# Optimization experiments

Measured on AMD Instinct MI355X. Metric: run time of the kernel, lower is better.

Reference implementation:

```python
import jax, jax.numpy as jnp
import numpy as np
import math

D = 768
H = 12
HD = D // H  # 64
B, N = 16, 1024
EPS = 1e-5


def _rope(x, cos, sin):
    # x: [B,N,H,hd]; cos,sin: [1,N,1,hd]
    x1, x2 = x[..., ::2], x[..., 1::2]
    return jnp.concatenate(
        [x1 * cos[..., ::2] - x2 * sin[..., ::2],
         x1 * sin[..., 1::2] + x2 * cos[..., 1::2]], axis=-1)


def setup_inputs() -> dict:
    key = jax.random.key(0)
    ks = jax.random.split(key, 8)
    s = 1.0 / math.sqrt(D)  # xavier-ish scale
    return {
        "x": jax.random.normal(ks[0], (B, N, D), jnp.float32),
        "rope_emb": jax.random.normal(ks[1], (N, HD), jnp.float32),
        "ln_w": jnp.ones((D,), jnp.float32),
        "ln_b": jnp.zeros((D,), jnp.float32),
        "enc_w": jax.random.normal(ks[2], (D, D), jnp.float32) * s,
        "enc_b": jnp.zeros((D,), jnp.float32),
        "qk_w": jax.random.normal(ks[3], (D, D), jnp.float32) * s,
        "qk_b": jnp.zeros((D,), jnp.float32),
        "v_w": jax.random.normal(ks[4], (D, D), jnp.float32) * s,
        "v_b": jnp.zeros((D,), jnp.float32),
        "out_w": jax.random.normal(ks[5], (D, D), jnp.float32) * s,
        "out_b": jnp.zeros((D,), jnp.float32),
        "gate_w": jax.random.normal(ks[6], (D, D), jnp.float32) * s,
        "gate_b": jnp.zeros((D,), jnp.float32),
    }


def reference(x, rope_emb, ln_w, ln_b, enc_w, enc_b, qk_w, qk_b,
              v_w, v_b, out_w, out_b, gate_w, gate_b):
    b, n, d = x.shape
    # Pre-LayerNorm
    mu = jnp.mean(x, axis=-1, keepdims=True)
    var = jnp.mean(jnp.square(x - mu), axis=-1, keepdims=True)
    x_norm = (x - mu) / jnp.sqrt(var + EPS) * ln_w + ln_b
    # sparse latent encoder
    x_latent = jax.nn.relu(x_norm @ enc_w.T + enc_b)
    qk = (x_latent @ qk_w.T + qk_b).reshape(b, n, H, HD)
    v = (x_latent @ v_w.T + v_b).reshape(b, n, H, HD)
    ang = rope_emb[:, :HD]
    cos = jnp.cos(ang)[None, :, None, :]
    sin = jnp.sin(ang)[None, :, None, :]
    qk = _rope(qk, cos, sin)
    # raw (softmax-free) attention, Q=K
    scores = jnp.einsum('bnhd,bmhd->bhnm', qk, qk) / math.sqrt(HD)
    attn = jnp.einsum('bhnm,bmhd->bnhd', scores, v).reshape(b, n, d)
    attn = attn @ out_w.T + out_b
    gate = jax.nn.sigmoid(x_norm @ gate_w.T + gate_b)
    return x + gate * attn
```

## Files before the change

kernel.cpp:

```cpp
#include <hip/hip_runtime.h>

typedef __bf16 bf16;
typedef __bf16 bf16x4 __attribute__((ext_vector_type(4)));
typedef __bf16 bf16x8 __attribute__((ext_vector_type(8)));
typedef float floatx4 __attribute__((ext_vector_type(4)));

#define DD 768
#define NH 12
#define HDIM 64
#define BB 16
#define NN 1024
#define MTOT (BB*NN)
#define WELEM (DD*DD)

__device__ __forceinline__ void async_cp16(const void* g, void* l) {
  __builtin_amdgcn_global_load_lds((const __attribute__((address_space(1))) void*)g,
                                   (__attribute__((address_space(3))) void*)l, 16, 0, 0);
}

__global__ __launch_bounds__(256) void ln_kernel(const float* __restrict__ x,
    const float* __restrict__ w, const float* __restrict__ b, bf16* __restrict__ A) {
  int row = blockIdx.x * 4 + (threadIdx.x >> 6);
  int lane = threadIdx.x & 63;
  const float4* xr = (const float4*)(x + (size_t)row * DD);
  float4 v[3];
  float s = 0.f;
#pragma unroll
  for (int i = 0; i < 3; i++) {
    v[i] = xr[lane + 64 * i];
    s += v[i].x + v[i].y + v[i].z + v[i].w;
  }
#pragma unroll
  for (int o = 32; o; o >>= 1) s += __shfl_xor(s, o);
  float mu = s * (1.f / 768.f);
  float vs = 0.f;
#pragma unroll
  for (int i = 0; i < 3; i++) {
    float dx;
    dx = v[i].x - mu; vs += dx * dx;
    dx = v[i].y - mu; vs += dx * dx;
    dx = v[i].z - mu; vs += dx * dx;
    dx = v[i].w - mu; vs += dx * dx;
  }
#pragma unroll
  for (int o = 32; o; o >>= 1) vs += __shfl_xor(vs, o);
  float rstd = rsqrtf(vs * (1.f / 768.f) + 1e-5f);
  const float4* wv = (const float4*)w;
  const float4* bv = (const float4*)b;
  bf16* Ar = A + (size_t)row * DD;
#pragma unroll
  for (int i = 0; i < 3; i++) {
    int c4 = lane + 64 * i;
    float4 ww = wv[c4], bb = bv[c4];
    bf16x4 pk;
    pk[0] = (bf16)((v[i].x - mu) * rstd * ww.x + bb.x);
    pk[1] = (bf16)((v[i].y - mu) * rstd * ww.y + bb.y);
    pk[2] = (bf16)((v[i].z - mu) * rstd * ww.z + bb.z);
    pk[3] = (bf16)((v[i].w - mu) * rstd * ww.w + bb.w);
    *(bf16x4*)(Ar + c4 * 4) = pk;
  }
}

__global__ __launch_bounds__(256) void convw_kernel(const float* __restrict__ w0,
    const float* __restrict__ w1, const float* __restrict__ w2,
    const float* __restrict__ w3, const float* __restrict__ w4, bf16* __restrict__ out) {
  int i = blockIdx.x * 256 + threadIdx.x;
  int which = i / (WELEM / 4);
  int off = (i % (WELEM / 4)) * 4;
  const float* s = which == 0 ? w0 : which == 1 ? w1 : which == 2 ? w2 : which == 3 ? w3 : w4;
  float4 v = *(const float4*)(s + off);
  bf16x4 pk;
  pk[0] = (bf16)v.x; pk[1] = (bf16)v.y; pk[2] = (bf16)v.z; pk[3] = (bf16)v.w;
  *(bf16x4*)(out + (size_t)i * 4) = pk;
}

template<int EPI>
__device__ __forceinline__ void gemm_body(
    int bm, int bn, int bnl,
    const bf16* __restrict__ Aop, const bf16* __restrict__ W,
    const float* __restrict__ bias,
    bf16* __restrict__ Cb, float* __restrict__ Cf,
    const float* __restrict__ Xres, const bf16* __restrict__ Gate,
    bf16* As, bf16* Bs) {
  int tid = threadIdx.x;
  int wave = tid >> 6, lane = tid & 63;
  int quad = lane >> 4, l16 = lane & 15;
  int wm = wave & 1, wn = wave >> 1;
  int sr = lane >> 3;
  int smcg = (lane & 7) ^ sr;

  const bf16* Ag = Aop + (size_t)(bm * 256) * DD;
  const bf16* Bg = W + (size_t)(bn * 128) * DD;

  floatx4 acc[8][4];
#pragma unroll
  for (int i = 0; i < 8; i++)
#pragma unroll
    for (int j = 0; j < 4; j++)
      acc[i][j] = (floatx4){0.f, 0.f, 0.f, 0.f};

  int swzA = (l16 & 7);

  for (int k0 = 0; k0 < DD; k0 += 64) {
    __syncthreads();
#pragma unroll
    for (int it = 0; it < 8; it++) {
      int c = it * 4 + wave;
      int row = c * 8 + sr;
      async_cp16(Ag + (size_t)row * DD + k0 + smcg * 8, &As[c * 512]);
    }
#pragma unroll
    for (int it = 0; it < 4; it++) {
      int c = it * 4 + wave;
      int row = c * 8 + sr;
      async_cp16(Bg + (size_t)row * DD + k0 + smcg * 8, &Bs[c * 512]);
    }
    __syncthreads();
#pragma unroll
    for (int ks = 0; ks < 2; ks++) {
      int cg = (ks * 4 + quad) ^ swzA;
      bf16x8 a[8], b[4];
#pragma unroll
      for (int i = 0; i < 8; i++) a[i] = *(const bf16x8*)&As[(wm * 128 + i * 16 + l16) * 64 + cg * 8];
#pragma unroll
      for (int i = 0; i < 4; i++) b[i] = *(const bf16x8*)&Bs[(wn * 64 + i * 16 + l16) * 64 + cg * 8];
      if (EPI == 2) {
#pragma unroll
        for (int mi = 0; mi < 8; mi++)
#pragma unroll
          for (int ni = 0; ni < 4; ni++)
            acc[mi][ni] = __builtin_amdgcn_mfma_f32_16x16x32_bf16(a[mi], b[ni], acc[mi][ni], 0, 0, 0);
      } else {
#pragma unroll
        for (int mi = 0; mi < 8; mi++)
#pragma unroll
          for (int ni = 0; ni < 4; ni++)
            acc[mi][ni] = __builtin_amdgcn_mfma_f32_16x16x32_bf16(b[ni], a[mi], acc[mi][ni], 0, 0, 0);
      }
    }
  }

  if (EPI == 2) {
#pragma unroll
    for (int ni = 0; ni < 4; ni++) {
      int gc = bnl * 128 + wn * 64 + ni * 16 + l16;
      float bz = bias[gc];
      int h = gc >> 6, dd2 = gc & 63;
#pragma unroll
      for (int mi = 0; mi < 8; mi++) {
        int gm0 = bm * 256 + wm * 128 + mi * 16 + quad * 4;
        int b_ = gm0 >> 10, n0 = gm0 & 1023;
        bf16x4 pk;
#pragma unroll
        for (int r = 0; r < 4; r++) pk[r] = (bf16)(acc[mi][ni][r] + bz);
        *(bf16x4*)&Cb[(((size_t)b_ * NH + h) * HDIM + dd2) * NN + n0] = pk;
      }
    }
  } else {
#pragma unroll
    for (int mi = 0; mi < 8; mi++) {
      int gm = bm * 256 + wm * 128 + mi * 16 + l16;
#pragma unroll
      for (int ni = 0; ni < 4; ni++) {
        int gc = bnl * 128 + wn * 64 + ni * 16 + quad * 4;
        float4 bz = *(const float4*)&bias[gc];
        float v0 = acc[mi][ni][0] + bz.x;
        float v1 = acc[mi][ni][1] + bz.y;
        float v2 = acc[mi][ni][2] + bz.z;
        float v3 = acc[mi][ni][3] + bz.w;
        size_t idx = (size_t)gm * DD + gc;
        if (EPI == 4) {
          bf16x4 g = *(const bf16x4*)&Gate[idx];
          float4 xr = *(const float4*)&Xres[idx];
          float4 o;
          o.x = xr.x + (float)g[0] * v0;
          o.y = xr.y + (float)g[1] * v1;
          o.z = xr.z + (float)g[2] * v2;
          o.w = xr.w + (float)g[3] * v3;
          *(float4*)&Cf[idx] = o;
        } else {
          bf16x4 pk;
          if (EPI == 0) {
            pk[0] = (bf16)fmaxf(v0, 0.f); pk[1] = (bf16)fmaxf(v1, 0.f);
            pk[2] = (bf16)fmaxf(v2, 0.f); pk[3] = (bf16)fmaxf(v3, 0.f);
          } else if (EPI == 1) {
            pk[0] = (bf16)v0; pk[1] = (bf16)v1; pk[2] = (bf16)v2; pk[3] = (bf16)v3;
          } else {
            pk[0] = (bf16)(1.f / (1.f + __expf(-v0)));
            pk[1] = (bf16)(1.f / (1.f + __expf(-v1)));
            pk[2] = (bf16)(1.f / (1.f + __expf(-v2)));
            pk[3] = (bf16)(1.f / (1.f + __expf(-v3)));
          }
          *(bf16x4*)&Cb[idx] = pk;
        }
      }
    }
  }
}

template<int EPI_LO, int EPI_HI, int NBN>
__global__ __launch_bounds__(256, 2) void gemm_kernel(
    const bf16* __restrict__ Aop, const bf16* __restrict__ W,
    const float* __restrict__ bias_lo, const float* __restrict__ bias_hi,
    bf16* __restrict__ C_lo, bf16* __restrict__ C_hi, float* __restrict__ Cf,
    const float* __restrict__ Xres, const bf16* __restrict__ Gate) {
  __shared__ bf16 As[256 * 64];
  __shared__ bf16 Bs[128 * 64];
  int blk = blockIdx.x;
  int xcd = blk & 7, slot = blk >> 3;
  int bm = xcd * 8 + slot / NBN;
  int bn = slot % NBN;
  if (NBN == 12 && bn >= 6) {
    gemm_body<EPI_HI>(bm, bn, bn - 6, Aop, W, bias_hi, C_hi, Cf, Xres, Gate, As, Bs);
  } else {
    gemm_body<EPI_LO>(bm, bn, bn, Aop, W, bias_lo, C_lo, Cf, Xres, Gate, As, Bs);
  }
}

#define TLS_S 132
__global__ __launch_bounds__(256) void rope_kernel(const bf16* __restrict__ QKraw,
    const float* __restrict__ rope, bf16* __restrict__ QKr, bf16* __restrict__ QKrT) {
  __shared__ bf16 Tls[64 * TLS_S];
  int blk = blockIdx.x;
  int bh = blk >> 3, nc = blk & 7;
  int b_ = bh / NH, h_ = bh % NH;
  int nbase = nc * 128;
  int t = threadIdx.x;
  {
    int n_loc = t >> 1, ch = t & 1;
    int n = nbase + n_loc;
    const bf16* src = QKraw + ((size_t)(b_ * NN + n)) * DD + h_ * HDIM + ch * 32;
    const float* rp = rope + n * HDIM + ch * 32;
    __attribute__((aligned(16))) bf16 o1[16];
    __attribute__((aligned(16))) bf16 o2[16];
#pragma unroll
    for (int i0 = 0; i0 < 4; i0++) {
      bf16x8 v = *(const bf16x8*)(src + i0 * 8);
      float4 r0 = *(const float4*)(rp + i0 * 8);
      float4 r1 = *(const float4*)(rp + i0 * 8 + 4);
      float a0s[4] = {r0.x, r0.z, r1.x, r1.z};
      float a1s[4] = {r0.y, r0.w, r1.y, r1.w};
#pragma unroll
      for (int p = 0; p < 4; p++) {
        float x1 = (float)v[2 * p], x2 = (float)v[2 * p + 1];
        float s0, c0, s1, c1;
        __sincosf(a0s[p], &s0, &c0);
        __sincosf(a1s[p], &s1, &c1);
        int d = i0 * 4 + p;
        o1[d] = (bf16)(x1 * c0 - x2 * s0);
        o2[d] = (bf16)(x1 * s1 + x2 * c1);
      }
    }
    bf16* dst = QKr + ((size_t)(b_ * NN + n)) * DD + h_ * HDIM;
    *(bf16x8*)&dst[ch * 16]      = *(bf16x8*)&o1[0];
    *(bf16x8*)&dst[ch * 16 + 8]  = *(bf16x8*)&o1[8];
    *(bf16x8*)&dst[32 + ch * 16]     = *(bf16x8*)&o2[0];
    *(bf16x8*)&dst[32 + ch * 16 + 8] = *(bf16x8*)&o2[8];
#pragma unroll
    for (int d = 0; d < 16; d++) {
      Tls[(ch * 16 + d) * TLS_S + n_loc] = o1[d];
      Tls[(32 + ch * 16 + d) * TLS_S + n_loc] = o2[d];
    }
  }
  __syncthreads();
  {
    int c = t >> 2, qn = t & 3;
    __attribute__((aligned(16))) bf16 buf[32];
#pragma unroll
    for (int j = 0; j < 8; j++)
      *(bf16x4*)&buf[j * 4] = *(const bf16x4*)&Tls[c * TLS_S + qn * 32 + j * 4];
    bf16* dst = QKrT + ((size_t)bh * HDIM + c) * NN + nbase + qn * 32;
#pragma unroll
    for (int j = 0; j < 4; j++)
      *(bf16x8*)&dst[j * 8] = *(bf16x8*)&buf[j * 8];
  }
}

__global__ __launch_bounds__(256) void attn_kernel(const bf16* __restrict__ QKr,
    const bf16* __restrict__ QKrT, const bf16* __restrict__ VT, bf16* __restrict__ attn) {
  __shared__ float Tp[64][64];
  __shared__ bf16 Tbf[64][72];
  int blk = blockIdx.x;
  int xcd = blk & 7, s = blk >> 3;
  int bhl = s >> 2, q = s & 3;
  int bh = xcd * 24 + bhl;
  int tid = threadIdx.x, wave = tid >> 6, lane = tid & 63;
  int quad = lane >> 4, l16 = lane & 15;
  const bf16* Qt = QKrT + (size_t)bh * (HDIM * NN);
  const bf16* Vt = VT + (size_t)bh * (HDIM * NN);

  floatx4 acc[4][4];
#pragma unroll
  for (int i = 0; i < 4; i++)
#pragma unroll
    for (int j = 0; j < 4; j++)
      acc[i][j] = (floatx4){0.f, 0.f, 0.f, 0.f};

  int kbase = wave * 256;
#pragma unroll
  for (int k0 = 0; k0 < 256; k0 += 32) {
    bf16x8 a[4], b[4];
#pragma unroll
    for (int i = 0; i < 4; i++) a[i] = *(const bf16x8*)&Qt[(size_t)(i * 16 + l16) * NN + kbase + k0 + quad * 8];
#pragma unroll
    for (int i = 0; i < 4; i++) b[i] = *(const bf16x8*)&Vt[(size_t)(i * 16 + l16) * NN + kbase + k0 + quad * 8];
#pragma unroll
    for (int mi = 0; mi < 4; mi++)
#pragma unroll
      for (int ni = 0; ni < 4; ni++)
        acc[mi][ni] = __builtin_amdgcn_mfma_f32_16x16x32_bf16(a[mi], b[ni], acc[mi][ni], 0, 0, 0);
  }
#pragma unroll
  for (int w = 0; w < 4; w++) {
    if (wave == w) {
#pragma unroll
      for (int mi = 0; mi < 4; mi++)
#pragma unroll
        for (int ni = 0; ni < 4; ni++)
#pragma unroll
          for (int r = 0; r < 4; r++) {
            float val = acc[mi][ni][r];
            float* p = &Tp[mi * 16 + quad * 4 + r][ni * 16 + l16];
            if (w == 0) *p = val; else *p += val;
          }
    }
    __syncthreads();
  }
  for (int e = tid; e < 4096; e += 256) {
    int d1 = e >> 6, d2 = e & 63;
    Tbf[d2][d1] = (bf16)(Tp[d1][d2] * 0.125f);
  }
  __syncthreads();

  int b_ = bh / NH, h_ = bh % NH;
  const bf16* Q = QKr + (size_t)(b_ * NN) * DD + h_ * HDIM;
  bf16* Ao = attn + (size_t)(b_ * NN) * DD + h_ * HDIM;
  bf16x8 Bf[4][2];
#pragma unroll
  for (int ni = 0; ni < 4; ni++)
#pragma unroll
    for (int ks = 0; ks < 2; ks++)
      Bf[ni][ks] = *(const bf16x8*)&Tbf[ni * 16 + l16][ks * 32 + quad * 8];

#pragma unroll
  for (int mi = 0; mi < 4; mi++) {
    int nrow = q * 256 + wave * 64 + mi * 16;
    bf16x8 a0 = *(const bf16x8*)&Q[(size_t)(nrow + l16) * DD + quad * 8];
    bf16x8 a1 = *(const bf16x8*)&Q[(size_t)(nrow + l16) * DD + 32 + quad * 8];
    floatx4 o[4];
#pragma unroll
    for (int ni = 0; ni < 4; ni++) o[ni] = (floatx4){0.f, 0.f, 0.f, 0.f};
#pragma unroll
    for (int ni = 0; ni < 4; ni++) {
      o[ni] = __builtin_amdgcn_mfma_f32_16x16x32_bf16(a0, Bf[ni][0], o[ni], 0, 0, 0);
      o[ni] = __builtin_amdgcn_mfma_f32_16x16x32_bf16(a1, Bf[ni][1], o[ni], 0, 0, 0);
    }
#pragma unroll
    for (int ni = 0; ni < 4; ni++)
#pragma unroll
      for (int r = 0; r < 4; r++)
        Ao[(size_t)(nrow + quad * 4 + r) * DD + ni * 16 + l16] = (bf16)o[ni][r];
  }
}

extern "C" void kernel_launch(void* const* d_in, const int* in_sizes, int n_in,
                              void* d_out, int out_size, void* d_ws, size_t ws_size,
                              hipStream_t stream) {
  const float* x      = (const float*)d_in[0];
  const float* rope   = (const float*)d_in[1];
  const float* ln_w   = (const float*)d_in[2];
  const float* ln_b   = (const float*)d_in[3];
  const float* enc_w  = (const float*)d_in[4];
  const float* enc_b  = (const float*)d_in[5];
  const float* qk_w   = (const float*)d_in[6];
  const float* qk_b   = (const float*)d_in[7];
  const float* v_w    = (const float*)d_in[8];
  const float* v_b    = (const float*)d_in[9];
  const float* out_w  = (const float*)d_in[10];
  const float* out_b  = (const float*)d_in[11];
  const float* gate_w = (const float*)d_in[12];
  const float* gate_b = (const float*)d_in[13];

  char* w = (char*)d_ws;
  const size_t S = (size_t)MTOT * DD * 2;
  bf16* s0 = (bf16*)(w);
  bf16* s1 = (bf16*)(w + S);
  bf16* s2 = (bf16*)(w + 2 * S);
  bf16* s3 = (bf16*)(w + 3 * S);
  bf16* s4 = (bf16*)(w + 4 * S);
  bf16* s5 = (bf16*)(w + 5 * S);
  bf16* Wb = (bf16*)(w + 6 * S);

  bf16* A = s0;
  bf16* L = s1;
  bf16* Gate = s2;
  bf16* QKraw = s0;
  bf16* QKr = s3;
  bf16* QKrT = s4;
  bf16* VT = s5;
  bf16* attnb = s1;

  ln_kernel<<<dim3(MTOT / 4), dim3(256), 0, stream>>>(x, ln_w, ln_b, A);
  convw_kernel<<<dim3(5 * WELEM / 4 / 256), dim3(256), 0, stream>>>(enc_w, gate_w, qk_w, v_w, out_w, Wb);

  gemm_kernel<0, 3, 12><<<dim3(768), dim3(256), 0, stream>>>(
      A, Wb, enc_b, gate_b, L, Gate, nullptr, nullptr, nullptr);
  gemm_kernel<1, 2, 12><<<dim3(768), dim3(256), 0, stream>>>(
      L, Wb + 2 * (size_t)WELEM, qk_b, v_b, QKraw, VT, nullptr, nullptr, nullptr);
  rope_kernel<<<dim3(BB * NH * 8), dim3(256), 0, stream>>>(QKraw, rope, QKr, QKrT);
  attn_kernel<<<dim3(BB * NH * 4), dim3(256), 0, stream>>>(QKr, QKrT, VT, attnb);
  gemm_kernel<4, 4, 6><<<dim3(384), dim3(256), 0, stream>>>(
      attnb, Wb + 4 * (size_t)WELEM, out_b, nullptr, nullptr, nullptr, (float*)d_out, x, Gate);
}
```

Before: 334.6 us.

## Triple-buffer GEMM K-loop with async LDS prefetch and 8-wave blocks

Rewrites the GEMM main loop as a 3-stage software pipeline. Global-to-LDS async copies for tile t+2 are issued while tile t is computed, with explicit vmcnt waits and raw s_barrier in place of the two __syncthreads per iteration. Blocks grow from 4 to 8 waves, each wave owning a 64x64 sub-tile instead of 128x64, and s_setprio is raised around the MFMA bursts. The goal is to hide global load latency and improve MFMA utilisation. In exchange LDS use triples to 144 KB per block, which may limit occupancy to one block per CU despite the launch bounds, and the hand-set waitcnt values must match the number of copies issued per stage.

```diff
diff --git a/kernel.cpp b/kernel.cpp
--- a/kernel.cpp
+++ b/kernel.cpp
@@ -12,6 +12,10 @@
 #define NN 1024
 #define MTOT (BB*NN)
 #define WELEM (DD*DD)
+
+#define ABUF 16384
+#define BBUF 8192
+#define TBUF (ABUF + BBUF)
 
 __device__ __forceinline__ void async_cp16(const void* g, void* l) {
   __builtin_amdgcn_global_load_lds((const __attribute__((address_space(1))) void*)g,
@@ -81,63 +85,77 @@
     const float* __restrict__ bias,
     bf16* __restrict__ Cb, float* __restrict__ Cf,
     const float* __restrict__ Xres, const bf16* __restrict__ Gate,
-    bf16* As, bf16* Bs) {
+    bf16* smem) {
   int tid = threadIdx.x;
-  int wave = tid >> 6, lane = tid & 63;
+  int w = tid >> 6, lane = tid & 63;
   int quad = lane >> 4, l16 = lane & 15;
-  int wm = wave & 1, wn = wave >> 1;
+  int wm = w >> 1, wn = w & 1;
   int sr = lane >> 3;
-  int smcg = (lane & 7) ^ sr;
+  int scg = (lane & 7) ^ sr;
+  int swz = l16 & 7;
 
   const bf16* Ag = Aop + (size_t)(bm * 256) * DD;
   const bf16* Bg = W + (size_t)(bn * 128) * DD;
-
-  floatx4 acc[8][4];
-#pragma unroll
-  for (int i = 0; i < 8; i++)
+  const bf16* srcA = Ag + (size_t)(w * 8 + sr) * DD + scg * 8;
+  const bf16* srcB = Bg + (size_t)(w * 8 + sr) * DD + scg * 8;
+
+  floatx4 acc[4][4];
+#pragma unroll
+  for (int i = 0; i < 4; i++)
 #pragma unroll
     for (int j = 0; j < 4; j++)
       acc[i][j] = (floatx4){0.f, 0.f, 0.f, 0.f};
 
-  int swzA = (l16 & 7);
-
-  for (int k0 = 0; k0 < DD; k0 += 64) {
-    __syncthreads();
-#pragma unroll
-    for (int it = 0; it < 8; it++) {
-      int c = it * 4 + wave;
-      int row = c * 8 + sr;
-      async_cp16(Ag + (size_t)row * DD + k0 + smcg * 8, &As[c * 512]);
-    }
-#pragma unroll
-    for (int it = 0; it < 4; it++) {
-      int c = it * 4 + wave;
-      int row = c * 8 + sr;
-      async_cp16(Bg + (size_t)row * DD + k0 + smcg * 8, &Bs[c * 512]);
-    }
-    __syncthreads();
+  auto stage = [&](int k0, bf16* buf) {
+#pragma unroll
+    for (int it = 0; it < 4; it++)
+      async_cp16(srcA + (size_t)it * (64 * DD) + k0, buf + (w + 8 * it) * 512);
+#pragma unroll
+    for (int jt = 0; jt < 2; jt++)
+      async_cp16(srcB + (size_t)jt * (64 * DD) + k0, buf + ABUF + (w + 8 * jt) * 512);
+  };
+
+  stage(0, smem);
+  stage(64, smem + TBUF);
+
+#pragma unroll
+  for (int t = 0; t < 12; t++) {
+    if (t + 2 < 12) stage((t + 2) * 64, smem + ((t + 2) % 3) * TBUF);
+    if (t < 10)       asm volatile("s_waitcnt vmcnt(12)" ::: "memory");
+    else if (t == 10) asm volatile("s_waitcnt vmcnt(6)" ::: "memory");
+    else              asm volatile("s_waitcnt vmcnt(0)" ::: "memory");
+    __builtin_amdgcn_s_barrier();
+    __builtin_amdgcn_sched_barrier(0);
+
+    const bf16* Ab = smem + (t % 3) * TBUF;
+    const bf16* Bb = Ab + ABUF;
 #pragma unroll
     for (int ks = 0; ks < 2; ks++) {
-      int cg = (ks * 4 + quad) ^ swzA;
-      bf16x8 a[8], b[4];
-#pragma unroll
-      for (int i = 0; i < 8; i++) a[i] = *(const bf16x8*)&As[(wm * 128 + i * 16 + l16) * 64 + cg * 8];
-#pragma unroll
-      for (int i = 0; i < 4; i++) b[i] = *(const bf16x8*)&Bs[(wn * 64 + i * 16 + l16) * 64 + cg * 8];
+      int cg = (ks * 4 + quad) ^ swz;
+      bf16x8 a[4], b[4];
+#pragma unroll
+      for (int i = 0; i < 4; i++) a[i] = *(const bf16x8*)&Ab[(wm * 64 + i * 16 + l16) * 64 + cg * 8];
+#pragma unroll
+      for (int i = 0; i < 4; i++) b[i] = *(const bf16x8*)&Bb[(wn * 64 + i * 16 + l16) * 64 + cg * 8];
+      __builtin_amdgcn_s_setprio(1);
       if (EPI == 2) {
 #pragma unroll
-        for (int mi = 0; mi < 8; mi++)
+        for (int mi = 0; mi < 4; mi++)
 #pragma unroll
           for (int ni = 0; ni < 4; ni++)
             acc[mi][ni] = __builtin_amdgcn_mfma_f32_16x16x32_bf16(a[mi], b[ni], acc[mi][ni], 0, 0, 0);
       } else {
 #pragma unroll
-        for (int mi = 0; mi < 8; mi++)
+        for (int mi = 0; mi < 4; mi++)
 #pragma unroll
           for (int ni = 0; ni < 4; ni++)
             acc[mi][ni] = __builtin_amdgcn_mfma_f32_16x16x32_bf16(b[ni], a[mi], acc[mi][ni], 0, 0, 0);
       }
-    }
+      __builtin_amdgcn_s_setprio(0);
+    }
+    asm volatile("s_waitcnt lgkmcnt(0)" ::: "memory");
+    __builtin_amdgcn_s_barrier();
+    __builtin_amdgcn_sched_barrier(0);
   }
 
   if (EPI == 2) {
@@ -147,8 +165,8 @@
       float bz = bias[gc];
       int h = gc >> 6, dd2 = gc & 63;
 #pragma unroll
-      for (int mi = 0; mi < 8; mi++) {
-        int gm0 = bm * 256 + wm * 128 + mi * 16 + quad * 4;
+      for (int mi = 0; mi < 4; mi++) {
+        int gm0 = bm * 256 + wm * 64 + mi * 16 + quad * 4;
         int b_ = gm0 >> 10, n0 = gm0 & 1023;
         bf16x4 pk;
 #pragma unroll
@@ -158,8 +176,8 @@
     }
   } else {
 #pragma unroll
-    for (int mi = 0; mi < 8; mi++) {
-      int gm = bm * 256 + wm * 128 + mi * 16 + l16;
+    for (int mi = 0; mi < 4; mi++) {
+      int gm = bm * 256 + wm * 64 + mi * 16 + l16;
 #pragma unroll
       for (int ni = 0; ni < 4; ni++) {
         int gc = bnl * 128 + wn * 64 + ni * 16 + quad * 4;
@@ -199,21 +217,20 @@
 }
 
 template<int EPI_LO, int EPI_HI, int NBN>
-__global__ __launch_bounds__(256, 2) void gemm_kernel(
+__global__ __launch_bounds__(512, 2) void gemm_kernel(
     const bf16* __restrict__ Aop, const bf16* __restrict__ W,
     const float* __restrict__ bias_lo, const float* __restrict__ bias_hi,
     bf16* __restrict__ C_lo, bf16* __restrict__ C_hi, float* __restrict__ Cf,
     const float* __restrict__ Xres, const bf16* __restrict__ Gate) {
-  __shared__ bf16 As[256 * 64];
-  __shared__ bf16 Bs[128 * 64];
+  __shared__ __attribute__((aligned(16))) bf16 smem[3 * TBUF];
   int blk = blockIdx.x;
   int xcd = blk & 7, slot = blk >> 3;
   int bm = xcd * 8 + slot / NBN;
   int bn = slot % NBN;
   if (NBN == 12 && bn >= 6) {
-    gemm_body<EPI_HI>(bm, bn, bn - 6, Aop, W, bias_hi, C_hi, Cf, Xres, Gate, As, Bs);
+    gemm_body<EPI_HI>(bm, bn, bn - 6, Aop, W, bias_hi, C_hi, Cf, Xres, Gate, smem);
   } else {
-    gemm_body<EPI_LO>(bm, bn, bn, Aop, W, bias_lo, C_lo, Cf, Xres, Gate, As, Bs);
+    gemm_body<EPI_LO>(bm, bn, bn, Aop, W, bias_lo, C_lo, Cf, Xres, Gate, smem);
   }
 }
 
@@ -403,12 +420,12 @@
   ln_kernel<<<dim3(MTOT / 4), dim3(256), 0, stream>>>(x, ln_w, ln_b, A);
   convw_kernel<<<dim3(5 * WELEM / 4 / 256), dim3(256), 0, stream>>>(enc_w, gate_w, qk_w, v_w, out_w, Wb);
 
-  gemm_kernel<0, 3, 12><<<dim3(768), dim3(256), 0, stream>>>(
+  gemm_kernel<0, 3, 12><<<dim3(768), dim3(512), 0, stream>>>(
       A, Wb, enc_b, gate_b, L, Gate, nullptr, nullptr, nullptr);
-  gemm_kernel<1, 2, 12><<<dim3(768), dim3(256), 0, stream>>>(
+  gemm_kernel<1, 2, 12><<<dim3(768), dim3(512), 0, stream>>>(
       L, Wb + 2 * (size_t)WELEM, qk_b, v_b, QKraw, VT, nullptr, nullptr, nullptr);
   rope_kernel<<<dim3(BB * NH * 8), dim3(256), 0, stream>>>(QKraw, rope, QKr, QKrT);
   attn_kernel<<<dim3(BB * NH * 4), dim3(256), 0, stream>>>(QKr, QKrT, VT, attnb);
-  gemm_kernel<4, 4, 6><<<dim3(384), dim3(256), 0, stream>>>(
+  gemm_kernel<4, 4, 6><<<dim3(384), dim3(512), 0, stream>>>(
       attnb, Wb + 4 * (size_t)WELEM, out_b, nullptr, nullptr, nullptr, (float*)d_out, x, Gate);
 }
```

After: 340.7 us. Within noise of the previous version (+1.8%).
